# Kernel optimization log

Measured on AMD Instinct MI355X. Metric: run time of the kernel, lower is better.

## Reference

```python
import jax, jax.numpy as jnp
import numpy as np

T = 500      # max_context_length (hard-coded in the original module)
D = 8192     # feature width of h / rows of c2q, q2c


def setup_inputs() -> dict:
    key = jax.random.key(0)
    k1, k2, k3 = jax.random.split(key, 3)
    h = jax.random.normal(k1, (1, T, D), dtype=jnp.float32)
    c2q = jax.random.normal(k2, (D, T), dtype=jnp.float32)
    q2c = jax.random.normal(k3, (D, T), dtype=jnp.float32)
    return {"h": h, "c2q": c2q, "q2c": q2c}


def reference(h, c2q, q2c):
    # Original loop builds, for each context position c:
    #   beta_c = concat([h[0,c], c2q.T[c], h[0,c]*c2q.T[c], h[0,c]*q2c.T[c]])  # [4D]
    # and stacks then transposes -> G of shape [4D, T].
    H = h[0]        # [T, D]
    C = c2q.T       # [T, D]
    Q = q2c.T       # [T, D]
    G = jnp.concatenate([H, C, H * C, H * Q], axis=1)  # [T, 4D]
    return G.T      # [4D, T]
```

## Files before the change

### kernel.cpp

```cpp
#include <hip/hip_runtime.h>
#include <hip/hip_bf16.h>

#define TCTX 500
#define DFEAT 8192
#define TD 32
#define TT 128
#define LDS_STRIDE (TT + 4)

__global__ __launch_bounds__(256) void MegaMerge_77283641524594_kernel(
    const float* __restrict__ h,
    const float* __restrict__ c2q,
    const float* __restrict__ q2c,
    float* __restrict__ out)
{
    __shared__ float hs[TD * LDS_STRIDE];

    const int tid = threadIdx.x;
    const int d0  = blockIdx.x * TD;
    const int t0  = blockIdx.y * TT;

    {
        const int dc = (tid & 7) * 4;
        const int tr = tid >> 3;
        #pragma unroll
        for (int it = 0; it < TT; it += 32) {
            const int t = t0 + tr + it;
            if (t < TCTX) {
                const float4 v = *reinterpret_cast<const float4*>(
                    &h[(size_t)t * DFEAT + d0 + dc]);
                const int tl = tr + it;
                hs[(dc + 0) * LDS_STRIDE + tl] = v.x;
                hs[(dc + 1) * LDS_STRIDE + tl] = v.y;
                hs[(dc + 2) * LDS_STRIDE + tl] = v.z;
                hs[(dc + 3) * LDS_STRIDE + tl] = v.w;
            }
        }
    }
    __syncthreads();

    const int t4 = tid & 31;
    const int t  = t0 + t4 * 4;
    if (t < TCTX) {
        #pragma unroll
        for (int dl = (tid >> 5); dl < TD; dl += 8) {
            const int j = d0 + dl;
            const float4 hv = *reinterpret_cast<const float4*>(
                &hs[dl * LDS_STRIDE + t4 * 4]);
            const float4 c = *reinterpret_cast<const float4*>(
                &c2q[(size_t)j * TCTX + t]);
            const float4 q = *reinterpret_cast<const float4*>(
                &q2c[(size_t)j * TCTX + t]);
            const float4 hc = make_float4(hv.x * c.x, hv.y * c.y,
                                          hv.z * c.z, hv.w * c.w);
            const float4 hq = make_float4(hv.x * q.x, hv.y * q.y,
                                          hv.z * q.z, hv.w * q.w);
            *reinterpret_cast<float4*>(&out[(size_t)j               * TCTX + t]) = hv;
            *reinterpret_cast<float4*>(&out[(size_t)(DFEAT + j)     * TCTX + t]) = c;
            *reinterpret_cast<float4*>(&out[(size_t)(2 * DFEAT + j) * TCTX + t]) = hc;
            *reinterpret_cast<float4*>(&out[(size_t)(3 * DFEAT + j) * TCTX + t]) = hq;
        }
    }
}

extern "C" void kernel_launch(void* const* d_in, const int* in_sizes, int n_in,
                              void* d_out, int out_size, void* d_ws, size_t ws_size,
                              hipStream_t stream) {
    const float* h   = (const float*)d_in[0];
    const float* c2q = (const float*)d_in[1];
    const float* q2c = (const float*)d_in[2];
    float* out = (float*)d_out;

    dim3 grid(DFEAT / TD, (TCTX + TT - 1) / TT);
    dim3 block(256);
    MegaMerge_77283641524594_kernel<<<grid, block, 0, stream>>>(h, c2q, q2c, out);
}
```

Baseline: 23.71 us.

## Cover full context per block and prefetch c2q/q2c before LDS transpose

Each block now handles 16 feature rows across the whole 500-long context using 512 threads, replacing the 2D grid of 32x128 tiles. The c2q and q2c float4 loads are issued into registers before the h transpose into shared memory, so their latency overlaps the LDS fill and barrier. This removes partial-tile waste along the context and raises the memory-level parallelism per thread. The cost is higher register pressure and 3 idle lanes per 128-thread row group; the LDS stride of 500 also changes the bank-conflict pattern for the transposed writes.

```diff
diff --git a/kernel.cpp b/kernel.cpp
--- a/kernel.cpp
+++ b/kernel.cpp
@@ -3,61 +3,71 @@
 
 #define TCTX 500
 #define DFEAT 8192
-#define TD 32
-#define TT 128
-#define LDS_STRIDE (TT + 4)
+#define BD 16
+#define LDS_S 500
 
-__global__ __launch_bounds__(256) void MegaMerge_77283641524594_kernel(
+__global__ __launch_bounds__(512) void MegaMerge_77283641524594_kernel(
     const float* __restrict__ h,
     const float* __restrict__ c2q,
     const float* __restrict__ q2c,
     float* __restrict__ out)
 {
-    __shared__ float hs[TD * LDS_STRIDE];
+    __shared__ float hs[BD * LDS_S];
 
     const int tid = threadIdx.x;
-    const int d0  = blockIdx.x * TD;
-    const int t0  = blockIdx.y * TT;
+    const int d0  = blockIdx.x * BD;
+
+    const int t4   = tid & 127;
+    const int rowg = tid >> 7;
+    const bool act = (t4 < 125);
+
+    float4 cpre[4], qpre[4];
+    if (act) {
+        #pragma unroll
+        for (int k = 0; k < 4; ++k) {
+            const size_t j = (size_t)(d0 + rowg + 4 * k);
+            cpre[k] = *reinterpret_cast<const float4*>(&c2q[j * TCTX + t4 * 4]);
+            qpre[k] = *reinterpret_cast<const float4*>(&q2c[j * TCTX + t4 * 4]);
+        }
+    }
 
     {
-        const int dc = (tid & 7) * 4;
-        const int tr = tid >> 3;
+        const int dc = (tid & 3) * 4;
+        const int tr = tid >> 2;
         #pragma unroll
-        for (int it = 0; it < TT; it += 32) {
-            const int t = t0 + tr + it;
+        for (int p = 0; p < 4; ++p) {
+            const int t = p * 128 + tr;
             if (t < TCTX) {
                 const float4 v = *reinterpret_cast<const float4*>(
                     &h[(size_t)t * DFEAT + d0 + dc]);
-                const int tl = tr + it;
-                hs[(dc + 0) * LDS_STRIDE + tl] = v.x;
-                hs[(dc + 1) * LDS_STRIDE + tl] = v.y;
-                hs[(dc + 2) * LDS_STRIDE + tl] = v.z;
-                hs[(dc + 3) * LDS_STRIDE + tl] = v.w;
+                hs[(dc + 0) * LDS_S + t] = v.x;
+                hs[(dc + 1) * LDS_S + t] = v.y;
+                hs[(dc + 2) * LDS_S + t] = v.z;
+                hs[(dc + 3) * LDS_S + t] = v.w;
             }
         }
     }
     __syncthreads();
 
-    const int t4 = tid & 31;
-    const int t  = t0 + t4 * 4;
-    if (t < TCTX) {
+    if (act) {
+        const size_t sec = (size_t)DFEAT * TCTX;
         #pragma unroll
-        for (int dl = (tid >> 5); dl < TD; dl += 8) {
-            const int j = d0 + dl;
+        for (int k = 0; k < 4; ++k) {
+            const int dl = rowg + 4 * k;
+            const size_t j = (size_t)(d0 + dl);
             const float4 hv = *reinterpret_cast<const float4*>(
-                &hs[dl * LDS_STRIDE + t4 * 4]);
-            const float4 c = *reinterpret_cast<const float4*>(
-                &c2q[(size_t)j * TCTX + t]);
-            const float4 q = *reinterpret_cast<const float4*>(
-                &q2c[(size_t)j * TCTX + t]);
+                &hs[dl * LDS_S + t4 * 4]);
+            const float4 c = cpre[k];
+            const float4 q = qpre[k];
             const float4 hc = make_float4(hv.x * c.x, hv.y * c.y,
                                           hv.z * c.z, hv.w * c.w);
             const float4 hq = make_float4(hv.x * q.x, hv.y * q.y,
                                           hv.z * q.z, hv.w * q.w);
-            *reinterpret_cast<float4*>(&out[(size_t)j               * TCTX + t]) = hv;
-            *reinterpret_cast<float4*>(&out[(size_t)(DFEAT + j)     * TCTX + t]) = c;
-            *reinterpret_cast<float4*>(&out[(size_t)(2 * DFEAT + j) * TCTX + t]) = hc;
-            *reinterpret_cast<float4*>(&out[(size_t)(3 * DFEAT + j) * TCTX + t]) = hq;
+            const size_t o = j * TCTX + t4 * 4;
+            *reinterpret_cast<float4*>(&out[o          ]) = hv;
+            *reinterpret_cast<float4*>(&out[o + sec    ]) = c;
+            *reinterpret_cast<float4*>(&out[o + 2 * sec]) = hc;
+            *reinterpret_cast<float4*>(&out[o + 3 * sec]) = hq;
         }
     }
 }
@@ -70,7 +80,7 @@
     const float* q2c = (const float*)d_in[2];
     float* out = (float*)d_out;
 
-    dim3 grid(DFEAT / TD, (TCTX + TT - 1) / TT);
-    dim3 block(256);
+    dim3 grid(DFEAT / BD);
+    dim3 block(512);
     MegaMerge_77283641524594_kernel<<<grid, block, 0, stream>>>(h, c2q, q2c, out);
 }
```

Measured after the change: 23.77 us. No clear change (+0.2%).
